# Kernel optimization log

Measured on AMD Instinct MI355X. Metric: run time of the kernel, lower is better.

## Reference

```python
import jax, jax.numpy as jnp
import numpy as np

N = 8192
TEMP = 0.5
EPS = 1e-12


def _normalize(z):
    # F.normalize(z, p=2, dim=1): x / max(||x||, eps)
    n = jnp.sqrt(jnp.sum(z * z, axis=1, keepdims=True))
    return z / jnp.maximum(n, EPS)


def _gcn(edge_index, edge_weight, x, w, b):
    # torch.sparse.mm(adj, x @ w): out[row] += adj[row, col] * support[col]
    support = x @ w
    msg = support[edge_index[1]] * edge_weight[:, None]
    return jax.ops.segment_sum(msg, edge_index[0], num_segments=N) + b


def _encoder(edge_index, edge_weight, feat, w_l1a, b_l1a, w_l1b, b_l1b, w_g1, b_g1, w_g2, b_g2):
    x = jax.nn.relu(feat @ w_l1a + b_l1a) @ w_l1b + b_l1b  # [N, 32]
    h = jax.nn.relu(_gcn(edge_index, edge_weight, x, w_g1, b_g1))  # [N, hid]
    return _gcn(edge_index, edge_weight, h, w_g2, b_g2)  # [N, act_fn]


def _proj(h, w_fc1, b_fc1, w_fc2, b_fc2):
    return jax.nn.elu(h @ w_fc1 + b_fc1) @ w_fc2 + b_fc2


def _loss(z1, z2):
    z1n = _normalize(z1)
    z2n = _normalize(z2)
    refl = jnp.exp((z1n @ z1n.T) / TEMP)      # [N, N]
    between = jnp.exp((z1n @ z2n.T) / TEMP)   # [N, N]
    denom = refl.sum(1) + between.sum(1) - jnp.diagonal(refl)
    return -jnp.log(jnp.diagonal(between) / denom)


def setup_inputs() -> dict:
    key = jax.random.key(0)
    ks = jax.random.split(key, 20)
    E = 262144
    in_dim, hid_dim, act_fn, out_dim = 512, 256, 128, 64

    def kaiming(k, shape):
        fan_in = shape[0]
        bound = np.sqrt(6.0 / fan_in)
        return jax.random.uniform(k, shape, jnp.float32, -bound, bound)

    return {
        "feat1": jax.random.normal(ks[0], (N, in_dim), jnp.float32),
        "feat2": jax.random.normal(ks[1], (N, in_dim), jnp.float32),
        "edge_index1": jax.random.randint(ks[2], (2, E), 0, N, jnp.int32),
        "edge_weight1": jax.random.uniform(ks[3], (E,), jnp.float32),
        "edge_index2": jax.random.randint(ks[4], (2, E), 0, N, jnp.int32),
        "edge_weight2": jax.random.uniform(ks[5], (E,), jnp.float32),
        "w_l1a": kaiming(ks[6], (in_dim, 64)),
        "b_l1a": jnp.zeros((64,), jnp.float32),
        "w_l1b": kaiming(ks[7], (64, 32)),
        "b_l1b": jnp.zeros((32,), jnp.float32),
        "w_g1": kaiming(ks[8], (32, hid_dim)),
        "b_g1": jnp.zeros((hid_dim,), jnp.float32),
        "w_g2": kaiming(ks[9], (hid_dim, act_fn)),
        "b_g2": jnp.zeros((act_fn,), jnp.float32),
        "w_fc1": kaiming(ks[10], (act_fn, out_dim)),
        "b_fc1": jnp.zeros((out_dim,), jnp.float32),
        "w_fc2": kaiming(ks[11], (out_dim, act_fn)),
        "b_fc2": jnp.zeros((act_fn,), jnp.float32),
    }


def reference(feat1, feat2, edge_index1, edge_weight1, edge_index2, edge_weight2,
              w_l1a, b_l1a, w_l1b, b_l1b, w_g1, b_g1, w_g2, b_g2,
              w_fc1, b_fc1, w_fc2, b_fc2):
    h1 = _encoder(edge_index1, edge_weight1, feat1, w_l1a, b_l1a, w_l1b, b_l1b, w_g1, b_g1, w_g2, b_g2)
    h2 = _encoder(edge_index2, edge_weight2, feat2, w_l1a, b_l1a, w_l1b, b_l1b, w_g1, b_g1, w_g2, b_g2)
    z1 = _proj(h1, w_fc1, b_fc1, w_fc2, b_fc2)
    z2 = _proj(h2, w_fc1, b_fc1, w_fc2, b_fc2)
    l1 = _loss(z1, z2)
    l2 = _loss(z2, z1)
    return ((l1 + l2) * 0.5).mean()
```

## Files before the change

### kernel.cpp

```cpp
#include <hip/hip_runtime.h>
#include <hip/hip_bf16.h>
#include <math.h>


#define NROWS 8192
#define MROWS 16384
#define NEDGE 262144
#define ECAP 128

typedef __attribute__((ext_vector_type(8))) short bf16x8;
typedef __attribute__((ext_vector_type(4))) float f32x4;
typedef __attribute__((ext_vector_type(2))) float f32x2;
typedef __attribute__((ext_vector_type(8))) int i32x8;
typedef long long i64;

__device__ __forceinline__ short f2bf(float f){
  union { float f; unsigned u; } cv; cv.f = f;
  unsigned u = cv.u;
  unsigned r = (u + 0x7fffu + ((u >> 16) & 1u)) >> 16;
  return (short)r;
}
__device__ __forceinline__ f32x4 mfma16(bf16x8 a, bf16x8 b, f32x4 c){
  return __builtin_amdgcn_mfma_f32_16x16x32_bf16(a, b, c, 0, 0, 0);
}
__device__ __forceinline__ float fexp2(float x){
#if __has_builtin(__builtin_amdgcn_exp2f)
  return __builtin_amdgcn_exp2f(x);
#else
  return exp2f(x);
#endif
}

template<int CTRL>
__device__ __forceinline__ float dpp_add(float v){
  int s = __builtin_amdgcn_update_dpp(0, __builtin_bit_cast(int, v),
                                      CTRL, 0xf, 0xf, true);
  return v + __builtin_bit_cast(float, s);
}
__device__ __forceinline__ float red16(float v){
  v = dpp_add<0x101>(v);
  v = dpp_add<0x102>(v);
  v = dpp_add<0x104>(v);
  v = dpp_add<0x108>(v);
  return v;
}

__device__ unsigned char f2e4m3_sw(float f){
  float a = fabsf(f);
  unsigned s = (__float_as_uint(f)>>24)&0x80u;
  if (!(a>0.f)) return (unsigned char)s;
  if (a>448.f) a=448.f;
  int e; frexpf(a,&e);
  int eff=e-1;
  unsigned code;
  if (eff<-6){
    float q=rintf(a*512.f);
    code=(unsigned)q; if(code>7)code=7;
  } else {
    float q=rintf(a*exp2f((float)(3-eff)));
    unsigned mant=(unsigned)q;
    if(mant>=16){mant=8;eff++;}
    if(eff>8) return (unsigned char)(s|0x7e);
    code=((unsigned)(eff+7)<<3)|(mant-8);
  }
  return (unsigned char)(s|code);
}
__device__ __forceinline__ unsigned short pack2fp8(float a, float b){
#if __has_builtin(__builtin_amdgcn_cvt_pk_fp8_f32)
  int v = __builtin_amdgcn_cvt_pk_fp8_f32(a, b, 0, false);
  return (unsigned short)(v & 0xffff);
#else
  return (unsigned short)((unsigned)f2e4m3_sw(a) | ((unsigned)f2e4m3_sw(b)<<8));
#endif
}

struct WtArgs {
  const float* src[6];
  short* dst[6];
  int K[6], N[6];
  int off[7];
  int nwt;
};
__global__ void setup_k(WtArgs a){
  int i = blockIdx.x*256 + threadIdx.x;
  if (i >= a.off[6]) return;
  int s = 0;
  #pragma unroll
  for (int j=1;j<6;j++) if (i >= a.off[j]) s=j;
  int l = i - a.off[s];
  int K=a.K[s], N=a.N[s];
  int k=l/N, n=l-k*N;
  a.dst[s][(long)n*K+k] = f2bf(a.src[s][l]);
}

__global__ __launch_bounds__(256) void fm2_k(const float* __restrict__ F0, const float* __restrict__ F1,
    const short* __restrict__ Wa, const float* __restrict__ ba,
    const short* __restrict__ Wb, const float* __restrict__ bb, short* __restrict__ xb,
    const int* __restrict__ ei1, const float* __restrict__ w1, int* __restrict__ deg1,
    int2* __restrict__ eg1,
    const int* __restrict__ ei2, const float* __restrict__ w2, int* __restrict__ deg2,
    int2* __restrict__ eg2){
  __shared__ short As[32*520];
  __shared__ short a1s[32*72];
  const int tid = threadIdx.x;
  if (blockIdx.x < 2*(NEDGE/256)){
    int b = blockIdx.x;
    bool g2 = (b >= NEDGE/256);
    const int* ei = g2 ? ei2 : ei1;
    const float* w = g2 ? w2 : w1;
    int* deg = g2 ? deg2 : deg1;
    int2* eg = g2 ? eg2 : eg1;
    int e = (b % (NEDGE/256))*256 + tid;
    int r = ei[e];
    int c = ei[NEDGE + e];
    float wv = w[e];
    int p = atomicAdd(&deg[r], 1);
    eg[(long)r*ECAP + p] = make_int2(c, __float_as_int(wv));
    return;
  }
  const int m0 = (blockIdx.x - 2*(NEDGE/256))*32;
  const float* F = (m0 < NROWS) ? (F0 + (long)m0*512) : (F1 + (long)(m0-NROWS)*512);
  {
    float4 st[16];
    #pragma unroll
    for (int i=0;i<16;i++) st[i] = *(const float4*)(F + (long)(i*256+tid)*4);
    #pragma unroll
    for (int i=0;i<16;i++){
      int idx = i*256+tid, row = idx>>7, c4 = idx&127;
      unsigned lo = (unsigned)(unsigned short)f2bf(st[i].x) | ((unsigned)(unsigned short)f2bf(st[i].y)<<16);
      unsigned hi = (unsigned)(unsigned short)f2bf(st[i].z) | ((unsigned)(unsigned short)f2bf(st[i].w)<<16);
      uint2 o = {lo, hi};
      *(uint2*)&As[row*520 + c4*4] = o;
    }
  }
  __syncthreads();
  const int wave = tid>>6, lane = tid&63, quad = lane>>4, cl = lane&15;
  f32x4 zero = {0.f,0.f,0.f,0.f};
  {
    const int wno = wave*16;
    f32x4 acc[2] = {zero, zero};
    #pragma unroll
    for (int kc=0;kc<16;kc++){
      const int ko = kc*32 + quad*8;
      bf16x8 a0 = *(const bf16x8*)&As[(cl)*520 + ko];
      bf16x8 a1 = *(const bf16x8*)&As[(16+cl)*520 + ko];
      bf16x8 b = *(const bf16x8*)(Wa + (long)(wno + cl)*512 + ko);
      acc[0] = mfma16(a0, b, acc[0]);
      acc[1] = mfma16(a1, b, acc[1]);
    }
    int col = wno + cl;
    float bv = ba[col];
    #pragma unroll
    for (int mt=0;mt<2;mt++)
      #pragma unroll
      for (int r=0;r<4;r++)
        a1s[(mt*16 + quad*4 + r)*72 + col] = f2bf(fmaxf(acc[mt][r] + bv, 0.f));
  }
  __syncthreads();
  if (wave < 2){
    f32x4 acc2[2] = {zero, zero};
    #pragma unroll
    for (int kc=0;kc<2;kc++){
      const int ko = kc*32 + quad*8;
      bf16x8 a = *(const bf16x8*)&a1s[(wave*16+cl)*72 + ko];
      #pragma unroll
      for (int nt=0;nt<2;nt++){
        bf16x8 b = *(const bf16x8*)(Wb + (long)(nt*16 + cl)*64 + ko);
        acc2[nt] = mfma16(a, b, acc2[nt]);
      }
    }
    #pragma unroll
    for (int nt=0;nt<2;nt++){
      int col = nt*16 + cl;
      float bv = bb[col];
      #pragma unroll
      for (int r=0;r<4;r++)
        xb[(long)(m0 + wave*16 + quad*4 + r)*32 + col] = f2bf(acc2[nt][r] + bv);
    }
  }
}

__device__ __forceinline__ void acc8(float* acc, int4 v, float f){
  const unsigned* u = (const unsigned*)&v;
  #pragma unroll
  for (int i=0;i<4;i++){
    union{unsigned x; float y;} lo, hi;
    lo.x = u[i] << 16;
    hi.x = u[i] & 0xffff0000u;
    acc[2*i]   = fmaf(f, lo.y, acc[2*i]);
    acc[2*i+1] = fmaf(f, hi.y, acc[2*i+1]);
  }
}
template<int C>
__device__ __forceinline__ void gather_row(float* acc, const short* sb,
                                           const int2* eg, int s, int e){
  int k = s;
  for (; k+16 <= e; k+=16){
    int2 cw[16]; int4 v[16];
    #pragma unroll
    for (int u=0;u<16;u++) cw[u] = eg[k+u];
    #pragma unroll
    for (int u=0;u<16;u++) v[u] = *(const int4*)(sb + (long)cw[u].x*C);
    #pragma unroll
    for (int u=0;u<16;u++) acc8(acc, v[u], __int_as_float(cw[u].y));
  }
  for (; k+4 <= e; k+=4){
    int2 c0=eg[k], c1=eg[k+1], c2=eg[k+2], c3=eg[k+3];
    int4 v0 = *(const int4*)(sb + (long)c0.x*C);
    int4 v1 = *(const int4*)(sb + (long)c1.x*C);
    int4 v2 = *(const int4*)(sb + (long)c2.x*C);
    int4 v3 = *(const int4*)(sb + (long)c3.x*C);
    acc8(acc,v0,__int_as_float(c0.y)); acc8(acc,v1,__int_as_float(c1.y));
    acc8(acc,v2,__int_as_float(c2.y)); acc8(acc,v3,__int_as_float(c3.y));
  }
  for (; k < e; k++){
    int2 c0 = eg[k];
    int4 v0 = *(const int4*)(sb + (long)c0.x*C);
    acc8(acc,v0,__int_as_float(c0.y));
  }
}

__global__ __launch_bounds__(256) void gg_k(const short* __restrict__ xb,
    const int* __restrict__ deg1, const int2* __restrict__ eg1,
    const int* __restrict__ deg2, const int2* __restrict__ eg2,
    const short* __restrict__ Wg1, const float* __restrict__ bg1,
    const short* __restrict__ Wg2, short* __restrict__ s2){
  __shared__ short axs[64*40];
  __shared__ short hbs[64*264];
  const int tid = threadIdx.x;
  const int m0 = blockIdx.x*64;
  {
    const int g = tid & 3, sub = tid >> 2;
    const int row = m0 + sub;
    const int* deg; const int2* eg; int soff, lr;
    if (row < NROWS){ deg=deg1; eg=eg1; soff=0; lr=row; }
    else            { deg=deg2; eg=eg2; soff=NROWS; lr=row-NROWS; }
    const short* sb = xb + (long)soff*32 + g*8;
    float acc[8];
    #pragma unroll
    for (int j=0;j<8;j++) acc[j] = 0.f;
    gather_row<32>(acc, sb, eg + (long)lr*ECAP, 0, deg[lr]);
    int4 ov;
    unsigned* ou = (unsigned*)&ov;
    #pragma unroll
    for (int i=0;i<4;i++)
      ou[i] = (unsigned)(unsigned short)f2bf(acc[2*i]) | ((unsigned)(unsigned short)f2bf(acc[2*i+1])<<16);
    *(int4*)&axs[sub*40 + g*8] = ov;
  }
  __syncthreads();
  const int wave = tid>>6, lane = tid&63, quad = lane>>4, cl = lane&15;
  f32x4 zero = {0.f,0.f,0.f,0.f};
  {
    const int wno = wave*64;
    f32x4 acc[4][4];
    #pragma unroll
    for (int i=0;i<4;i++)
      #pragma unroll
      for (int j=0;j<4;j++) acc[i][j]=zero;
    const int ko = quad*8;
    bf16x8 a[4], b[4];
    #pragma unroll
    for (int mt=0;mt<4;mt++)
      a[mt] = *(const bf16x8*)&axs[(mt*16+cl)*40 + ko];
    #pragma unroll
    for (int nt=0;nt<4;nt++)
      b[nt] = *(const bf16x8*)(Wg1 + (long)(wno + nt*16 + cl)*32 + ko);
    #pragma unroll
    for (int mt=0;mt<4;mt++)
      #pragma unroll
      for (int nt=0;nt<4;nt++)
        acc[mt][nt] = mfma16(a[mt], b[nt], acc[mt][nt]);
    #pragma unroll
    for (int nt=0;nt<4;nt++){
      int col = wno + nt*16 + cl;
      float bv = bg1[col];
      #pragma unroll
      for (int mt=0;mt<4;mt++)
        #pragma unroll
        for (int r=0;r<4;r++)
          hbs[(mt*16 + quad*4 + r)*264 + col] = f2bf(fmaxf(acc[mt][nt][r] + bv, 0.f));
    }
  }
  __syncthreads();
  {
    const int wno = wave*32;
    f32x4 acc[4][2];
    #pragma unroll
    for (int i=0;i<4;i++){ acc[i][0]=zero; acc[i][1]=zero; }
    #pragma unroll
    for (int kc=0;kc<8;kc++){
      const int ko = kc*32 + quad*8;
      bf16x8 a[4], b[2];
      #pragma unroll
      for (int mt=0;mt<4;mt++)
        a[mt] = *(const bf16x8*)&hbs[(mt*16+cl)*264 + ko];
      #pragma unroll
      for (int nt=0;nt<2;nt++)
        b[nt] = *(const bf16x8*)(Wg2 + (long)(wno + nt*16 + cl)*256 + ko);
      #pragma unroll
      for (int mt=0;mt<4;mt++)
        #pragma unroll
        for (int nt=0;nt<2;nt++)
          acc[mt][nt] = mfma16(a[mt], b[nt], acc[mt][nt]);
    }
    #pragma unroll
    for (int mt=0;mt<4;mt++)
      #pragma unroll
      for (int nt=0;nt<2;nt++){
        int col = wno + nt*16 + cl;
        #pragma unroll
        for (int r=0;r<4;r++)
          s2[(long)(m0 + mt*16 + quad*4 + r)*128 + col] = f2bf(acc[mt][nt][r]);
      }
  }
}

__global__ __launch_bounds__(256) void pn_k(const short* __restrict__ s2,
    const int* __restrict__ deg1, const int2* __restrict__ eg1,
    const int* __restrict__ deg2, const int2* __restrict__ eg2,
    const float* __restrict__ bg2,
    const short* __restrict__ Wf1, const float* __restrict__ bf1,
    const short* __restrict__ Wf2, const float* __restrict__ bf2,
    unsigned short* __restrict__ Zf, float* __restrict__ bdot){
  __shared__ short hs[64*136];
  __shared__ short t2s[64*72];
  __shared__ float zs[64*132];
  __shared__ float sp[4][64];
  __shared__ float dp[4][32];
  __shared__ float rnS[64];
  const float SQKE = 1.6986436f;
  const int tid = threadIdx.x;
  const int wave = tid>>6, lane = tid&63, quad = lane>>4, cl = lane&15;
  const int m0h = blockIdx.x*32;
  {
    const int g = tid & 15, sub = tid >> 4;
    #pragma unroll 1
    for (int pass=0; pass<4; pass++){
      int hrow = pass*16 + sub;
      int lr = m0h + (hrow & 31);
      const int* deg; const int2* eg; long soff;
      if (hrow < 32){ deg=deg1; eg=eg1; soff=0; }
      else          { deg=deg2; eg=eg2; soff=NROWS; }
      const short* sb = s2 + soff*128 + g*8;
      float acc[8];
      #pragma unroll
      for (int j=0;j<8;j++) acc[j] = bg2[g*8+j];
      gather_row<128>(acc, sb, eg + (long)lr*ECAP, 0, deg[lr]);
      int4 ov;
      unsigned* ou = (unsigned*)&ov;
      #pragma unroll
      for (int i=0;i<4;i++)
        ou[i] = (unsigned)(unsigned short)f2bf(acc[2*i]) | ((unsigned)(unsigned short)f2bf(acc[2*i+1])<<16);
      *(int4*)&hs[hrow*136 + g*8] = ov;
    }
  }
  __syncthreads();
  f32x4 zero = {0.f,0.f,0.f,0.f};
  {
    const int wno = wave*16;
    f32x4 acc[4];
    #pragma unroll
    for (int i=0;i<4;i++) acc[i]=zero;
    #pragma unroll
    for (int kc=0;kc<4;kc++){
      const int ko = kc*32 + quad*8;
      bf16x8 a[4], b;
      #pragma unroll
      for (int mt=0;mt<4;mt++)
        a[mt] = *(const bf16x8*)&hs[(mt*16+cl)*136 + ko];
      b = *(const bf16x8*)(Wf1 + (long)(wno + cl)*128 + ko);
      #pragma unroll
      for (int mt=0;mt<4;mt++) acc[mt] = mfma16(a[mt], b, acc[mt]);
    }
    int col = wno + cl;
    float bv = bf1[col];
    #pragma unroll
    for (int mt=0;mt<4;mt++)
      #pragma unroll
      for (int r=0;r<4;r++){
        float v = acc[mt][r] + bv;
        v = (v > 0.f) ? v : expm1f(v);
        t2s[(mt*16 + quad*4 + r)*72 + col] = f2bf(v);
      }
  }
  __syncthreads();
  {
    const int wno = wave*32;
    f32x4 acc[4][2];
    #pragma unroll
    for (int i=0;i<4;i++){ acc[i][0]=zero; acc[i][1]=zero; }
    #pragma unroll
    for (int kc=0;kc<2;kc++){
      const int ko = kc*32 + quad*8;
      bf16x8 a[4], b[2];
      #pragma unroll
      for (int mt=0;mt<4;mt++)
        a[mt] = *(const bf16x8*)&t2s[(mt*16+cl)*72 + ko];
      #pragma unroll
      for (int nt=0;nt<2;nt++)
        b[nt] = *(const bf16x8*)(Wf2 + (long)(wno + nt*16 + cl)*64 + ko);
      #pragma unroll
      for (int mt=0;mt<4;mt++)
        #pragma unroll
        for (int nt=0;nt<2;nt++)
          acc[mt][nt] = mfma16(a[mt], b[nt], acc[mt][nt]);
    }
    #pragma unroll
    for (int mt=0;mt<4;mt++)
      #pragma unroll
      for (int nt=0;nt<2;nt++){
        int col = wno + nt*16 + cl;
        float bv = bf2[col];
        #pragma unroll
        for (int r=0;r<4;r++)
          zs[(mt*16 + quad*4 + r)*132 + col] = acc[mt][nt][r] + bv;
      }
  }
  __syncthreads();
  {
    int row = tid & 63, qtr = tid >> 6;
    const float* zr = &zs[row*132 + qtr*32];
    float s = 0.f;
    #pragma unroll 8
    for (int c=0;c<32;c++) s += zr[c]*zr[c];
    sp[qtr][row] = s;
    if (row < 32){
      const float* zb_ = &zs[(row+32)*132 + qtr*32];
      float d = 0.f;
      #pragma unroll 8
      for (int c=0;c<32;c++) d += zr[c]*zb_[c];
      dp[qtr][row] = d;
    }
  }
  __syncthreads();
  if (tid < 64){
    float ssq = sp[0][tid]+sp[1][tid]+sp[2][tid]+sp[3][tid];
    rnS[tid] = 1.f / fmaxf(sqrtf(ssq), 1e-12f);
  }
  __syncthreads();
  if (tid < 32){
    float dot = dp[0][tid]+dp[1][tid]+dp[2][tid]+dp[3][tid];
    bdot[m0h + tid] = dot * rnS[tid] * rnS[tid+32];
  }
  {
    int lr = tid >> 2;
    int grow = (lr < 32) ? (m0h + lr) : (NROWS + m0h + lr - 32);
    float s = rnS[lr] * SQKE;
    int p0 = (tid & 3)*16;
    long gbase = (long)(grow>>4)*1024 + (long)(grow&15)*16 + (long)(p0>>4)*256;
    #pragma unroll
    for (int pp=0;pp<16;pp++){
      int p = p0 + pp;
      Zf[gbase + pp] = pack2fp8(zs[lr*132 + 2*p]*s, zs[lr*132 + 2*p + 1]*s);
    }
  }
}

__global__ __launch_bounds__(256,4) void gram3_k(const unsigned char* __restrict__ Zf,
                                                 float* __restrict__ P){
  __shared__ float srow[4][64];
  __shared__ float scol[4][64];
  const int wave = threadIdx.x>>6, lane = threadIdx.x&63;
  const int t = blockIdx.x*4 + wave;
  int ti = (int)((513.0f - sqrtf(513.0f*513.0f - 8.0f*(float)t))*0.5f);
  while ((ti+1)*256 - ((ti+1)*ti)/2 <= t) ti++;
  while (ti*256 - (ti*(ti-1))/2 > t) ti--;
  const int tj = ti + (t - (ti*256 - (ti*(ti-1))/2));
  const unsigned char* za = Zf + (long)ti*8192 + lane*32;
  const unsigned char* zb = Zf + (long)tj*8192 + lane*32;
  const int quad = lane>>4, cl = lane&15;

  f32x4 zero = {0.f,0.f,0.f,0.f};
  f32x2 z2 = {0.f,0.f};
  f32x2 cs[4] = {z2,z2,z2,z2};

  i32x8 Bf[4];
  #pragma unroll
  for (int nt=0;nt<4;nt++)
    Bf[nt] = *(const i32x8*)(zb + nt*2048);

  i32x8 Ab[2];
  Ab[0] = *(const i32x8*)(za);
  Ab[1] = *(const i32x8*)(za + 2048);

  auto exprow = [&](const f32x4* ar, int mt){
    f32x2 r01 = z2, r23 = z2;
    #pragma unroll
    for (int nt=0;nt<4;nt++){
      f32x4 v = ar[nt];
      float e0 = fexp2(v[0]), e1 = fexp2(v[1]);
      float e2 = fexp2(v[2]), e3 = fexp2(v[3]);
      f32x2 p01 = {e0,e1}, p23 = {e2,e3};
      r01 += p01; r23 += p23;
      cs[nt] += p01; cs[nt] += p23;
    }
    float s0 = red16(r01.x);
    float s1 = red16(r01.y);
    float s2 = red16(r23.x);
    float s3 = red16(r23.y);
    if (cl==0){
      f32x4 rv = {s0, s1, s2, s3};
      *(f32x4*)&srow[wave][mt*16 + quad*4] = rv;
    }
  };

  const int SC1 = 0x7F;
  f32x4 acc2[2][4];
  #pragma unroll
  for (int nt=0;nt<4;nt++)
    acc2[0][nt] = __builtin_amdgcn_mfma_scale_f32_16x16x128_f8f6f4(
        Ab[0], Bf[nt], zero, 0, 0, 0, SC1, 0, SC1);
  #pragma unroll
  for (int mt=1; mt<4; mt++){
    const int cur = mt&1, prv = cur^1;
    if (mt<3)
      Ab[prv] = *(const i32x8*)(za + (mt+1)*2048);
    #pragma unroll
    for (int nt=0;nt<4;nt++)
      acc2[cur][nt] = __builtin_amdgcn_mfma_scale_f32_16x16x128_f8f6f4(
          Ab[cur], Bf[nt], zero, 0, 0, 0, SC1, 0, SC1);
    exprow(&acc2[prv][0], mt-1);
  }
  exprow(&acc2[1][0], 3);

  __threadfence_block();
  P[((long)ti*256 + tj)*64 + lane] = srow[wave][lane];
  if (ti != tj){
    #pragma unroll
    for (int nt=0;nt<4;nt++){
      float s = cs[nt].x + cs[nt].y;
      s += __shfl_xor(s,16); s += __shfl_xor(s,32);
      if (quad==0) scol[wave][nt*16 + cl] = s;
    }
    __threadfence_block();
    P[((long)tj*256 + ti)*64 + lane] = scol[wave][lane];
  }
}

__global__ __launch_bounds__(256) void rloss_k(const float* __restrict__ P,
                                               const float* __restrict__ bdot,
                                               float* __restrict__ out){
  __shared__ float ps[8][32][2];
  const float E2 = 7.3890560989306495f;
  int t = threadIdx.x;
  int rloc = t & 31, grp = t >> 5;
  int i = blockIdx.x*32 + rloc;
  int j = i + NROWS;
  const float* p1 = P + (long)(i>>6)*256*64 + (long)grp*32*64 + (i&63);
  const float* p2 = P + (long)(j>>6)*256*64 + (long)grp*32*64 + (j&63);
  float s1 = 0.f, s2 = 0.f;
  #pragma unroll 8
  for (int b=0;b<32;b++){ s1 += p1[b*64]; s2 += p2[b*64]; }
  ps[grp][rloc][0] = s1;
  ps[grp][rloc][1] = s2;
  __syncthreads();
  if (t < 64){
    float term = 0.f;
    if (t < 32){
      float a1 = 0.f, a2 = 0.f;
      #pragma unroll
      for (int g=0; g<8; g++){ a1 += ps[g][t][0]; a2 += ps[g][t][1]; }
      int ii = blockIdx.x*32 + t;
      float lb = 2.f * bdot[ii];
      term = 0.5f * ((logf(a1 - E2) - lb) + (logf(a2 - E2) - lb));
    }
    #pragma unroll
    for (int m=1; m<64; m<<=1) term += __shfl_xor(term, m);
    if (t==0) atomicAdd(out, term / (float)NROWS);
  }
}

extern "C" void kernel_launch(void* const* d_in, const int* in_sizes, int n_in,
                              void* d_out, int out_size, void* d_ws, size_t ws_size,
                              hipStream_t stream){
  const float* feat1 = (const float*)d_in[0];
  const float* feat2 = (const float*)d_in[1];
  const int*   ei1   = (const int*)d_in[2];
  const float* w1    = (const float*)d_in[3];
  const int*   ei2   = (const int*)d_in[4];
  const float* w2    = (const float*)d_in[5];
  const float* w_l1a = (const float*)d_in[6];
  const float* b_l1a = (const float*)d_in[7];
  const float* w_l1b = (const float*)d_in[8];
  const float* b_l1b = (const float*)d_in[9];
  const float* w_g1  = (const float*)d_in[10];
  const float* b_g1  = (const float*)d_in[11];
  const float* w_g2  = (const float*)d_in[12];
  const float* b_g2  = (const float*)d_in[13];
  const float* w_fc1 = (const float*)d_in[14];
  const float* b_fc1 = (const float*)d_in[15];
  const float* w_fc2 = (const float*)d_in[16];
  const float* b_fc2 = (const float*)d_in[17];

  float* P = (float*)d_ws;
  char* base = (char*)d_ws;
  size_t off = (size_t)17<<20;
  auto alloc = [&](size_t bytes)->void*{
    void* r = base + off;
    off = (off + bytes + 255) & ~(size_t)255;
    return r;
  };
  short* xb   = (short*)alloc((size_t)MROWS*32*2);
  short* s2   = (short*)alloc((size_t)MROWS*128*2);
  short* wl1a_t = (short*)alloc(512*64*2);
  short* wl1b_t = (short*)alloc(64*32*2);
  short* wg1_t  = (short*)alloc(32*256*2);
  short* wg2_t  = (short*)alloc(256*128*2);
  short* wfc1_t = (short*)alloc(128*64*2);
  short* wfc2_t = (short*)alloc(64*128*2);
  unsigned short* Zf = (unsigned short*)alloc((size_t)MROWS*128);
  int*   deg1 = (int*)alloc(NROWS*4);
  int*   deg2 = (int*)alloc(NROWS*4);
  int2*  eg1 = (int2*)alloc((size_t)NROWS*ECAP*8);
  int2*  eg2 = (int2*)alloc((size_t)NROWS*ECAP*8);
  float* bdot  = (float*)alloc(NROWS*4);

  hipMemsetAsync(deg1, 0, (size_t)2*NROWS*4, stream);
  hipMemsetAsync(d_out, 0, sizeof(float), stream);

  WtArgs wa;
  wa.src[0]=w_l1a; wa.dst[0]=wl1a_t; wa.K[0]=512; wa.N[0]=64;
  wa.src[1]=w_l1b; wa.dst[1]=wl1b_t; wa.K[1]=64;  wa.N[1]=32;
  wa.src[2]=w_g1;  wa.dst[2]=wg1_t;  wa.K[2]=32;  wa.N[2]=256;
  wa.src[3]=w_g2;  wa.dst[3]=wg2_t;  wa.K[3]=256; wa.N[3]=128;
  wa.src[4]=w_fc1; wa.dst[4]=wfc1_t; wa.K[4]=128; wa.N[4]=64;
  wa.src[5]=w_fc2; wa.dst[5]=wfc2_t; wa.K[5]=64;  wa.N[5]=128;
  wa.off[0]=0;
  for (int i=0;i<6;i++) wa.off[i+1] = wa.off[i] + wa.K[i]*wa.N[i];
  wa.nwt = (wa.off[6]+255)/256;

  setup_k<<<wa.nwt,256,0,stream>>>(wa);
  fm2_k<<<2*(NEDGE/256) + MROWS/32,256,0,stream>>>(feat1, feat2, wl1a_t, b_l1a,
      wl1b_t, b_l1b, xb,
      ei1, w1, deg1, eg1,
      ei2, w2, deg2, eg2);
  gg_k<<<MROWS/64,256,0,stream>>>(xb, deg1,eg1, deg2,eg2,
                                  wg1_t, b_g1, wg2_t, s2);
  pn_k<<<NROWS/32,256,0,stream>>>(s2, deg1,eg1, deg2,eg2, b_g2,
                                  wfc1_t, b_fc1, wfc2_t, b_fc2, Zf, bdot);
  gram3_k<<<8224,256,0,stream>>>((const unsigned char*)Zf, P);
  rloss_k<<<NROWS/32,256,0,stream>>>(P, bdot, (float*)d_out);
}
```

Before: 221.0 us.

## Shrink row tiles in GCN kernels and split edge gathers across threads

The first GCN kernel now processes 16 rows per block instead of 64. Each row's edge list is split across four thread groups, whose partial sums are reduced through shared memory before the MFMA stages. The second kernel halves its rows per block from 32 to 16 node pairs. Both changes launch more blocks and spread the latency-bound gather over more threads. The cost is less weight reuse per block and more redundant weight loads from global memory.

Result: no change. 219.0 us (-0.9%).

```diff
diff --git a/kernel.cpp b/kernel.cpp
--- a/kernel.cpp
+++ b/kernel.cpp
@@ -225,93 +225,88 @@
     const int* __restrict__ deg2, const int2* __restrict__ eg2,
     const short* __restrict__ Wg1, const float* __restrict__ bg1,
     const short* __restrict__ Wg2, short* __restrict__ s2){
-  __shared__ short axs[64*40];
-  __shared__ short hbs[64*264];
+  __shared__ short axs[16*40];
+  __shared__ short hbs[16*264];
+  __shared__ float tmp[16][4][3][8];
   const int tid = threadIdx.x;
-  const int m0 = blockIdx.x*64;
-  {
-    const int g = tid & 3, sub = tid >> 2;
+  const int m0 = blockIdx.x*16;
+  {
+    const int g = tid & 3, h = (tid>>2)&3, sub = tid >> 4;
     const int row = m0 + sub;
     const int* deg; const int2* eg; int soff, lr;
     if (row < NROWS){ deg=deg1; eg=eg1; soff=0; lr=row; }
     else            { deg=deg2; eg=eg2; soff=NROWS; lr=row-NROWS; }
     const short* sb = xb + (long)soff*32 + g*8;
+    int d = deg[lr];
+    int st = (d*h)>>2, en = (d*(h+1))>>2;
     float acc[8];
     #pragma unroll
     for (int j=0;j<8;j++) acc[j] = 0.f;
-    gather_row<32>(acc, sb, eg + (long)lr*ECAP, 0, deg[lr]);
-    int4 ov;
-    unsigned* ou = (unsigned*)&ov;
-    #pragma unroll
-    for (int i=0;i<4;i++)
-      ou[i] = (unsigned)(unsigned short)f2bf(acc[2*i]) | ((unsigned)(unsigned short)f2bf(acc[2*i+1])<<16);
-    *(int4*)&axs[sub*40 + g*8] = ov;
+    gather_row<32>(acc, sb, eg + (long)lr*ECAP, st, en);
+    if (h > 0){
+      #pragma unroll
+      for (int j=0;j<8;j++) tmp[sub][g][h-1][j] = acc[j];
+    }
+    __syncthreads();
+    if (h == 0){
+      #pragma unroll
+      for (int j=0;j<8;j++)
+        acc[j] = ((acc[j] + tmp[sub][g][0][j]) + tmp[sub][g][1][j]) + tmp[sub][g][2][j];
+      int4 ov;
+      unsigned* ou = (unsigned*)&ov;
+      #pragma unroll
+      for (int i=0;i<4;i++)
+        ou[i] = (unsigned)(unsigned short)f2bf(acc[2*i]) | ((unsigned)(unsigned short)f2bf(acc[2*i+1])<<16);
+      *(int4*)&axs[sub*40 + g*8] = ov;
+    }
   }
   __syncthreads();
   const int wave = tid>>6, lane = tid&63, quad = lane>>4, cl = lane&15;
   f32x4 zero = {0.f,0.f,0.f,0.f};
   {
     const int wno = wave*64;
-    f32x4 acc[4][4];
-    #pragma unroll
-    for (int i=0;i<4;i++)
-      #pragma unroll
-      for (int j=0;j<4;j++) acc[i][j]=zero;
+    f32x4 acc[4];
+    #pragma unroll
+    for (int i=0;i<4;i++) acc[i]=zero;
     const int ko = quad*8;
-    bf16x8 a[4], b[4];
-    #pragma unroll
-    for (int mt=0;mt<4;mt++)
-      a[mt] = *(const bf16x8*)&axs[(mt*16+cl)*40 + ko];
+    bf16x8 a0 = *(const bf16x8*)&axs[cl*40 + ko];
+    bf16x8 b[4];
     #pragma unroll
     for (int nt=0;nt<4;nt++)
       b[nt] = *(const bf16x8*)(Wg1 + (long)(wno + nt*16 + cl)*32 + ko);
     #pragma unroll
-    for (int mt=0;mt<4;mt++)
-      #pragma unroll
-      for (int nt=0;nt<4;nt++)
-        acc[mt][nt] = mfma16(a[mt], b[nt], acc[mt][nt]);
+    for (int nt=0;nt<4;nt++)
+      acc[nt] = mfma16(a0, b[nt], acc[nt]);
     #pragma unroll
     for (int nt=0;nt<4;nt++){
       int col = wno + nt*16 + cl;
       float bv = bg1[col];
       #pragma unroll
-      for (int mt=0;mt<4;mt++)
-        #pragma unroll
-        for (int r=0;r<4;r++)
-          hbs[(mt*16 + quad*4 + r)*264 + col] = f2bf(fmaxf(acc[mt][nt][r] + bv, 0.f));
+      for (int r=0;r<4;r++)
+        hbs[(quad*4 + r)*264 + col] = f2bf(fmaxf(acc[nt][r] + bv, 0.f));
     }
   }
   __syncthreads();
   {
     const int wno = wave*32;
-    f32x4 acc[4][2];
-    #pragma unroll
-    for (int i=0;i<4;i++){ acc[i][0]=zero; acc[i][1]=zero; }
+    f32x4 acc[2] = {zero, zero};
     #pragma unroll
     for (int kc=0;kc<8;kc++){
       const int ko = kc*32 + quad*8;
-      bf16x8 a[4], b[2];
-      #pragma unroll
-      for (int mt=0;mt<4;mt++)
-        a[mt] = *(const bf16x8*)&hbs[(mt*16+cl)*264 + ko];
-      #pragma unroll
-      for (int nt=0;nt<2;nt++)
-        b[nt] = *(const bf16x8*)(Wg2 + (long)(wno + nt*16 + cl)*256 + ko);
-      #pragma unroll
-      for (int mt=0;mt<4;mt++)
-        #pragma unroll
-        for (int nt=0;nt<2;nt++)
-          acc[mt][nt] = mfma16(a[mt], b[nt], acc[mt][nt]);
-    }
-    #pragma unroll
-    for (int mt=0;mt<4;mt++)
+      bf16x8 a = *(const bf16x8*)&hbs[cl*264 + ko];
       #pragma unroll
       for (int nt=0;nt<2;nt++){
-        int col = wno + nt*16 + cl;
-        #pragma unroll
-        for (int r=0;r<4;r++)
-          s2[(long)(m0 + mt*16 + quad*4 + r)*128 + col] = f2bf(acc[mt][nt][r]);
+        bf16x8 b = *(const bf16x8*)(Wg2 + (long)(wno + nt*16 + cl)*256 + ko);
+        acc[nt] = mfma16(a, b, acc[nt]);
       }
+    }
+    #pragma unroll
+    for (int nt=0;nt<2;nt++){
+      int col = wno + nt*16 + cl;
+      #pragma unroll
+      for (int r=0;r<4;r++)
+        s2[(long)(m0 + quad*4 + r)*128 + col] = f2bf(acc[nt][r]);
+    }
   }
 }
 
@@ -322,24 +317,24 @@
     const short* __restrict__ Wf1, const float* __restrict__ bf1,
     const short* __restrict__ Wf2, const float* __restrict__ bf2,
     unsigned short* __restrict__ Zf, float* __restrict__ bdot){
-  __shared__ short hs[64*136];
-  __shared__ short t2s[64*72];
-  __shared__ float zs[64*132];
-  __shared__ float sp[4][64];
-  __shared__ float dp[4][32];
-  __shared__ float rnS[64];
+  __shared__ short hs[32*136];
+  __shared__ short t2s[32*72];
+  __shared__ float zs[32*132];
+  __shared__ float sp[8][32];
+  __shared__ float dp[8][16];
+  __shared__ float rnS[32];
   const float SQKE = 1.6986436f;
   const int tid = threadIdx.x;
   const int wave = tid>>6, lane = tid&63, quad = lane>>4, cl = lane&15;
-  const int m0h = blockIdx.x*32;
+  const int m0h = blockIdx.x*16;
   {
     const int g = tid & 15, sub = tid >> 4;
     #pragma unroll 1
-    for (int pass=0; pass<4; pass++){
+    for (int pass=0; pass<2; pass++){
       int hrow = pass*16 + sub;
-      int lr = m0h + (hrow & 31);
+      int lr = m0h + (hrow & 15);
       const int* deg; const int2* eg; long soff;
-      if (hrow < 32){ deg=deg1; eg=eg1; soff=0; }
+      if (hrow < 16){ deg=deg1; eg=eg1; soff=0; }
       else          { deg=deg2; eg=eg2; soff=NROWS; }
       const short* sb = s2 + soff*128 + g*8;
       float acc[8];
@@ -358,24 +353,22 @@
   f32x4 zero = {0.f,0.f,0.f,0.f};
   {
     const int wno = wave*16;
-    f32x4 acc[4];
-    #pragma unroll
-    for (int i=0;i<4;i++) acc[i]=zero;
+    f32x4 acc[2] = {zero, zero};
     #pragma unroll
     for (int kc=0;kc<4;kc++){
       const int ko = kc*32 + quad*8;
-      bf16x8 a[4], b;
-      #pragma unroll
-      for (int mt=0;mt<4;mt++)
+      bf16x8 a[2], b;
+      #pragma unroll
+      for (int mt=0;mt<2;mt++)
         a[mt] = *(const bf16x8*)&hs[(mt*16+cl)*136 + ko];
       b = *(const bf16x8*)(Wf1 + (long)(wno + cl)*128 + ko);
       #pragma unroll
-      for (int mt=0;mt<4;mt++) acc[mt] = mfma16(a[mt], b, acc[mt]);
+      for (int mt=0;mt<2;mt++) acc[mt] = mfma16(a[mt], b, acc[mt]);
     }
     int col = wno + cl;
     float bv = bf1[col];
     #pragma unroll
-    for (int mt=0;mt<4;mt++)
+    for (int mt=0;mt<2;mt++)
       #pragma unroll
       for (int r=0;r<4;r++){
         float v = acc[mt][r] + bv;
@@ -386,27 +379,27 @@
   __syncthreads();
   {
     const int wno = wave*32;
-    f32x4 acc[4][2];
-    #pragma unroll
-    for (int i=0;i<4;i++){ acc[i][0]=zero; acc[i][1]=zero; }
+    f32x4 acc[2][2];
+    #pragma unroll
+    for (int i=0;i<2;i++){ acc[i][0]=zero; acc[i][1]=zero; }
     #pragma unroll
     for (int kc=0;kc<2;kc++){
       const int ko = kc*32 + quad*8;
-      bf16x8 a[4], b[2];
-      #pragma unroll
-      for (int mt=0;mt<4;mt++)
+      bf16x8 a[2], b[2];
+      #pragma unroll
+      for (int mt=0;mt<2;mt++)
         a[mt] = *(const bf16x8*)&t2s[(mt*16+cl)*72 + ko];
       #pragma unroll
       for (int nt=0;nt<2;nt++)
         b[nt] = *(const bf16x8*)(Wf2 + (long)(wno + nt*16 + cl)*64 + ko);
       #pragma unroll
-      for (int mt=0;mt<4;mt++)
+      for (int mt=0;mt<2;mt++)
         #pragma unroll
         for (int nt=0;nt<2;nt++)
           acc[mt][nt] = mfma16(a[mt], b[nt], acc[mt][nt]);
     }
     #pragma unroll
-    for (int mt=0;mt<4;mt++)
+    for (int mt=0;mt<2;mt++)
       #pragma unroll
       for (int nt=0;nt<2;nt++){
         int col = wno + nt*16 + cl;
@@ -418,38 +411,41 @@
   }
   __syncthreads();
   {
-    int row = tid & 63, qtr = tid >> 6;
-    const float* zr = &zs[row*132 + qtr*32];
+    int row = tid & 31, qtr = tid >> 5;
+    const float* zr = &zs[row*132 + qtr*16];
     float s = 0.f;
     #pragma unroll 8
-    for (int c=0;c<32;c++) s += zr[c]*zr[c];
+    for (int c=0;c<16;c++) s += zr[c]*zr[c];
     sp[qtr][row] = s;
-    if (row < 32){
-      const float* zb_ = &zs[(row+32)*132 + qtr*32];
+    if (row < 16){
+      const float* zb_ = &zs[(row+16)*132 + qtr*16];
       float d = 0.f;
       #pragma unroll 8
-      for (int c=0;c<32;c++) d += zr[c]*zb_[c];
+      for (int c=0;c<16;c++) d += zr[c]*zb_[c];
       dp[qtr][row] = d;
     }
   }
   __syncthreads();
-  if (tid < 64){
-    float ssq = sp[0][tid]+sp[1][tid]+sp[2][tid]+sp[3][tid];
+  if (tid < 32){
+    float ssq = ((sp[0][tid]+sp[1][tid])+(sp[2][tid]+sp[3][tid]))
+              + ((sp[4][tid]+sp[5][tid])+(sp[6][tid]+sp[7][tid]));
     rnS[tid] = 1.f / fmaxf(sqrtf(ssq), 1e-12f);
   }
   __syncthreads();
-  if (tid < 32){
-    float dot = dp[0][tid]+dp[1][tid]+dp[2][tid]+dp[3][tid];
-    bdot[m0h + tid] = dot * rnS[tid] * rnS[tid+32];
-  }
-  {
-    int lr = tid >> 2;
-    int grow = (lr < 32) ? (m0h + lr) : (NROWS + m0h + lr - 32);
+  if (tid < 16){
+    float dot = ((dp[0][tid]+dp[1][tid])+(dp[2][tid]+dp[3][tid]))
+              + ((dp[4][tid]+dp[5][tid])+(dp[6][tid]+dp[7][tid]));
+    bdot[m0h + tid] = dot * rnS[tid] * rnS[tid+16];
+  }
+  {
+    int lr = tid >> 3;
+    int grow = (lr < 16) ? (m0h + lr) : (NROWS + m0h + lr - 16);
     float s = rnS[lr] * SQKE;
-    int p0 = (tid & 3)*16;
-    long gbase = (long)(grow>>4)*1024 + (long)(grow&15)*16 + (long)(p0>>4)*256;
-    #pragma unroll
-    for (int pp=0;pp<16;pp++){
+    int p0 = (tid & 7)*8;
+    long gbase = (long)(grow>>4)*1024 + (long)(p0>>4)*256
+               + (long)(grow&15)*16 + (p0&15);
+    #pragma unroll
+    for (int pp=0;pp<8;pp++){
       int p = p0 + pp;
       Zf[gbase + pp] = pack2fp8(zs[lr*132 + 2*p]*s, zs[lr*132 + 2*p + 1]*s);
     }
@@ -634,9 +630,9 @@
       wl1b_t, b_l1b, xb,
       ei1, w1, deg1, eg1,
       ei2, w2, deg2, eg2);
-  gg_k<<<MROWS/64,256,0,stream>>>(xb, deg1,eg1, deg2,eg2,
+  gg_k<<<MROWS/16,256,0,stream>>>(xb, deg1,eg1, deg2,eg2,
                                   wg1_t, b_g1, wg2_t, s2);
-  pn_k<<<NROWS/32,256,0,stream>>>(s2, deg1,eg1, deg2,eg2, b_g2,
+  pn_k<<<NROWS/16,256,0,stream>>>(s2, deg1,eg1, deg2,eg2, b_g2,
                                   wfc1_t, b_fc1, wfc2_t, b_fc2, Zf, bdot);
   gram3_k<<<8224,256,0,stream>>>((const unsigned char*)Zf, P);
   rloss_k<<<NROWS/32,256,0,stream>>>(P, bdot, (float*)d_out);
```
